# Kernel optimization log

Measured on AMD Instinct MI355X. Metric: run time of the kernel, lower is better.

## Reference

```python
import jax, jax.numpy as jnp
import numpy as np

EMB_DIM = 768
HEAD = 12
HEAD_DIM = EMB_DIM // HEAD


def setup_inputs() -> dict:
    key = jax.random.key(0)
    ks = jax.random.split(key, 6)
    B, N, D = 8, 1024, EMB_DIM
    s = 1.0 / np.sqrt(D)
    return {
        "z": jax.random.normal(ks[0], (B, N, D), dtype=jnp.float32),
        "w_q": jax.random.normal(ks[1], (D, D), dtype=jnp.float32) * s,
        "w_k": jax.random.normal(ks[2], (D, D), dtype=jnp.float32) * s,
        "w_v": jax.random.normal(ks[3], (D, D), dtype=jnp.float32) * s,
        "w_o": jax.random.normal(ks[4], (D, D), dtype=jnp.float32) * s,
        "b_o": jax.random.normal(ks[5], (D,), dtype=jnp.float32) * 0.01,
    }


def reference(z, w_q, w_k, w_v, w_o, b_o):
    B, N, D = z.shape
    sqrt_dh = jnp.asarray(HEAD_DIM, z.dtype) ** 0.5
    # project and split heads: [B, H, N, Dh]
    def heads(x, w):
        return (x @ w.T).reshape(B, N, HEAD, HEAD_DIM).transpose(0, 2, 1, 3)
    q = heads(z, w_q)
    k = heads(z, w_k)
    v = heads(z, w_v)
    dots = jnp.einsum("bhqd,bhkd->bhqk", q, k) / sqrt_dh
    attn = jax.nn.softmax(dots, axis=-1)  # dropout p=0 -> identity
    out = jnp.einsum("bhqk,bhkd->bhqd", attn, v)
    out = out.transpose(0, 2, 1, 3).reshape(B, N, D)
    return out @ w_o.T + b_o
```

## Files before the change

kernel.cpp:

```cpp
#include <hip/hip_runtime.h>
#include <hip/hip_bf16.h>
#include <stdint.h>

typedef unsigned short u16;
typedef __attribute__((ext_vector_type(8))) short bf16x8;
typedef __attribute__((ext_vector_type(4))) float f32x4;

__device__ __forceinline__ u16 f2bf(float f) {
    union { float f; unsigned int i; } c; c.f = f;
    unsigned int x = c.i;
    return (u16)((x + 0x7FFFu + ((x >> 16) & 1u)) >> 16);
}
__device__ __forceinline__ u16 f2bf_fast(float f) {
    union { float f; unsigned int i; } c; c.f = f;
    return (u16)((c.i + 0x8000u) >> 16);
}

__device__ __forceinline__ void glds16(const u16* g, u16* l) {
    __builtin_amdgcn_global_load_lds(
        (const __attribute__((address_space(1))) void*)g,
        (__attribute__((address_space(3))) void*)l, 16, 0, 0);
}

__global__ __launch_bounds__(256) void convert_all(
    const float* __restrict__ z, const float* __restrict__ wq,
    const float* __restrict__ wk, const float* __restrict__ wv,
    const float* __restrict__ wo,
    u16* __restrict__ zb, u16* __restrict__ wqb, u16* __restrict__ wkb,
    u16* __restrict__ wvb, u16* __restrict__ wob)
{
    int g = blockIdx.x * 256 + threadIdx.x;
    const float* s; u16* d;
    if (g < 786432)       { s = z;  d = zb;  }
    else if (g < 860160)  { s = wq; d = wqb; g -= 786432; }
    else if (g < 933888)  { s = wk; d = wkb; g -= 860160; }
    else if (g < 1007616) { s = wv; d = wvb; g -= 933888; }
    else                  { s = wo; d = wob; g -= 1007616; }
    float4 a = *(const float4*)(s + (size_t)g * 8);
    float4 b = *(const float4*)(s + (size_t)g * 8 + 4);
    u16 t[8] = {f2bf(a.x), f2bf(a.y), f2bf(a.z), f2bf(a.w),
                f2bf(b.x), f2bf(b.y), f2bf(b.z), f2bf(b.w)};
    *(uint4*)(d + (size_t)g * 8) = *(const uint4*)t;
}

__device__ __forceinline__ void gemm_mainloop(
    const u16* __restrict__ A, const u16* __restrict__ B,
    u16* As, u16* Bs, f32x4 (&acc)[4][4], int m0, int lda, int ldb, int K)
{
    const int t = threadIdx.x;
    const int w = t >> 6, lane = t & 63, quad = lane >> 4, lc = lane & 15;
    const int wm = w >> 1, wn = w & 1;
    const int c0 = (2 * w) * 64 + lane, c1 = c0 + 64;
    const int kq0 = c0 >> 7, row0 = c0 & 127;
    const int kq1 = c1 >> 7, row1 = c1 & 127;

    const u16* a0 = &A[(size_t)(m0 + row0) * lda + kq0 * 8];
    const u16* a1 = &A[(size_t)(m0 + row1) * lda + kq1 * 8];
    const u16* b0 = &B[(size_t)row0 * ldb + kq0 * 8];
    const u16* b1 = &B[(size_t)row1 * ldb + kq1 * 8];
    u16* la0 = &As[(2 * w) * 512];        u16* la1 = la0 + 512;
    u16* lb0 = &Bs[(2 * w) * 512];        u16* lb1 = lb0 + 512;

    glds16(a0, la0);  glds16(a1, la1);
    glds16(b0, lb0);  glds16(b1, lb1);
    __syncthreads();

    int buf = 0;
    for (int k0 = 0; k0 < K; k0 += 32) {
        if (k0 + 32 < K) {
            const int nb = (buf ^ 1) * 4096;
            glds16(a0 + k0 + 32, la0 + nb);  glds16(a1 + k0 + 32, la1 + nb);
            glds16(b0 + k0 + 32, lb0 + nb);  glds16(b1 + k0 + 32, lb1 + nb);
        }
        bf16x8 af[4], bfr[4];
        #pragma unroll
        for (int i = 0; i < 4; i++)
            af[i]  = *(const bf16x8*)&As[buf * 4096 + (quad * 128 + 64 * wm + 16 * i + lc) * 8];
        #pragma unroll
        for (int j = 0; j < 4; j++)
            bfr[j] = *(const bf16x8*)&Bs[buf * 4096 + (quad * 128 + 64 * wn + 16 * j + lc) * 8];
        #pragma unroll
        for (int i = 0; i < 4; i++)
            #pragma unroll
            for (int j = 0; j < 4; j++)
                acc[i][j] = __builtin_amdgcn_mfma_f32_16x16x32_bf16(af[i], bfr[j], acc[i][j], 0, 0, 0);
        __syncthreads();
        buf ^= 1;
    }
}

__global__ __launch_bounds__(256) void qkv_gemm(
    const u16* __restrict__ zb, const u16* __restrict__ wqb,
    const u16* __restrict__ wkb, const u16* __restrict__ wvb,
    u16* __restrict__ qkb, u16* __restrict__ vt)
{
    __shared__ __align__(16) u16 As[8192], Bs[8192];
    const int n0 = blockIdx.x * 128, m0 = blockIdx.y * 128;
    const u16* B;
    if (n0 < 768)       B = wqb + (size_t)n0 * 768;
    else if (n0 < 1536) B = wkb + (size_t)(n0 - 768) * 768;
    else                B = wvb + (size_t)(n0 - 1536) * 768;

    f32x4 acc[4][4] = {};
    gemm_mainloop(zb, B, As, Bs, acc, m0, 768, 768, 768);

    const int t = threadIdx.x;
    const int w = t >> 6, lane = t & 63, quad = lane >> 4, lc = lane & 15;
    const int wm = w >> 1, wn = w & 1;

    if (n0 < 1536) {
        #pragma unroll
        for (int i = 0; i < 4; i++)
            #pragma unroll
            for (int j = 0; j < 4; j++) {
                const int col = n0 + 64 * wn + 16 * j + lc;
                #pragma unroll
                for (int r = 0; r < 4; r++) {
                    const int row = m0 + 64 * wm + 16 * i + quad * 4 + r;
                    qkb[(size_t)row * 1536 + col] = f2bf_fast(acc[i][j][r]);
                }
            }
    } else {
        #pragma unroll
        for (int i = 0; i < 4; i++)
            #pragma unroll
            for (int j = 0; j < 4; j++) {
                const int c = (n0 - 1536) + 64 * wn + 16 * j + lc;
                const int h = c >> 6, d = c & 63;
                const int tok0 = m0 + 64 * wm + 16 * i + quad * 4;
                const int b = tok0 >> 10, n = tok0 & 1023;
                ushort4 pk = { f2bf_fast(acc[i][j][0]), f2bf_fast(acc[i][j][1]),
                               f2bf_fast(acc[i][j][2]), f2bf_fast(acc[i][j][3]) };
                *(ushort4*)&vt[(((size_t)(b * 12 + h)) * 64 + d) * 1024 + n] = pk;
            }
    }
}

__global__ __launch_bounds__(256) void oproj_gemm(
    const u16* __restrict__ ob, const u16* __restrict__ wob,
    const float* __restrict__ bo, float* __restrict__ out)
{
    __shared__ __align__(16) u16 As[8192], Bs[8192];
    const int n0 = blockIdx.x * 128, m0 = blockIdx.y * 128;
    f32x4 acc[4][4] = {};
    gemm_mainloop(ob, wob + (size_t)n0 * 768, As, Bs, acc, m0, 768, 768, 768);

    const int t = threadIdx.x;
    const int w = t >> 6, lane = t & 63, quad = lane >> 4, lc = lane & 15;
    const int wm = w >> 1, wn = w & 1;
    #pragma unroll
    for (int i = 0; i < 4; i++)
        #pragma unroll
        for (int j = 0; j < 4; j++) {
            const int col = n0 + 64 * wn + 16 * j + lc;
            const float bv = bo[col];
            #pragma unroll
            for (int r = 0; r < 4; r++) {
                const int row = m0 + 64 * wm + 16 * i + quad * 4 + r;
                out[(size_t)row * 768 + col] = acc[i][j][r] + bv;
            }
        }
}

__global__ __launch_bounds__(512, 4) void attn_kernel(
    const u16* __restrict__ qkb, const u16* __restrict__ vt,
    u16* __restrict__ obuf)
{
    const int b = blockIdx.x / 12, h = blockIdx.x % 12;
    const int q0 = blockIdx.y * 128;
    const int t = threadIdx.x;
    const int w = t >> 6, lane = t & 63, quad = lane >> 4, lc = lane & 15;

    const u16* Qp  = qkb + (size_t)b * 1024 * 1536 + h * 64;
    const u16* Kp  = Qp + 768;
    const u16* Vtp = vt + ((size_t)(b * 12 + h)) * 64 * 1024;

    __shared__ __align__(16) u16 U[128 * 136];
    __shared__ __align__(16) u16 Vts[64 * 128];

    bf16x8 qf[2];
    #pragma unroll
    for (int kk = 0; kk < 2; kk++)
        qf[kk] = *(const bf16x8*)&Qp[(size_t)(q0 + 16 * w + lc) * 1536 + kk * 32 + quad * 8];

    f32x4 oacc[4] = {};
    float lsum[4] = {0.0f, 0.0f, 0.0f, 0.0f};

    const float cs = 0.18033688011112042f;

    for (int kt = 0; kt < 8; kt++) {
        const int kb = kt * 128;
        __syncthreads();
        #pragma unroll
        for (int s2 = 0; s2 < 2; s2++) {
            const int s = 2 * w + s2;
            const int c = s * 64 + lane;
            const int kq = c >> 7, row = c & 127;
            glds16(&Kp[(size_t)(kb + row) * 1536 + kq * 8], &U[s * 512]);
        }
        #pragma unroll
        for (int s2 = 0; s2 < 2; s2++) {
            const int s = 2 * w + s2;
            const int c = s * 64 + lane;
            const int d = c >> 4, kq = (c & 15) ^ (d & 15);
            glds16(&Vtp[(size_t)d * 1024 + kb + kq * 8], &Vts[s * 512]);
        }
        __syncthreads();

        f32x4 sacc[8] = {};
        #pragma unroll
        for (int j = 0; j < 8; j++) {
            bf16x8 kf0 = *(const bf16x8*)&U[((quad) * 128 + 16 * j + lc) * 8];
            bf16x8 kf1 = *(const bf16x8*)&U[((4 + quad) * 128 + 16 * j + lc) * 8];
            sacc[j] = __builtin_amdgcn_mfma_f32_16x16x32_bf16(qf[0], kf0, sacc[j], 0, 0, 0);
            sacc[j] = __builtin_amdgcn_mfma_f32_16x16x32_bf16(qf[1], kf1, sacc[j], 0, 0, 0);
        }
        __syncthreads();

        #pragma unroll
        for (int j = 0; j < 8; j++)
            #pragma unroll
            for (int r = 0; r < 4; r++) {
                float p = __builtin_amdgcn_exp2f(sacc[j][r] * cs);
                lsum[r] += p;
                U[(16 * w + quad * 4 + r) * 136 + 16 * j + lc] = f2bf_fast(p);
            }

        #pragma unroll
        for (int ks = 0; ks < 4; ks++) {
            bf16x8 pa = *(const bf16x8*)&U[(16 * w + lc) * 136 + ks * 32 + quad * 8];
            #pragma unroll
            for (int jd = 0; jd < 4; jd++) {
                bf16x8 vb = *(const bf16x8*)&Vts[(((16 * jd + lc) << 4) + ((ks * 4 + quad) ^ lc)) * 8];
                oacc[jd] = __builtin_amdgcn_mfma_f32_16x16x32_bf16(pa, vb, oacc[jd], 0, 0, 0);
            }
        }
    }

    #pragma unroll
    for (int off = 1; off < 16; off <<= 1)
        #pragma unroll
        for (int r = 0; r < 4; r++)
            lsum[r] += __shfl_xor(lsum[r], off, 64);

    float invl[4];
    #pragma unroll
    for (int r = 0; r < 4; r++) invl[r] = __builtin_amdgcn_rcpf(lsum[r]);
    #pragma unroll
    for (int jd = 0; jd < 4; jd++)
        #pragma unroll
        for (int r = 0; r < 4; r++) {
            const int row = q0 + 16 * w + quad * 4 + r;
            const int col = h * 64 + 16 * jd + lc;
            obuf[((size_t)b * 1024 + row) * 768 + col] = f2bf_fast(oacc[jd][r] * invl[r]);
        }
}

extern "C" void kernel_launch(void* const* d_in, const int* in_sizes, int n_in,
                              void* d_out, int out_size, void* d_ws, size_t ws_size,
                              hipStream_t stream) {
    const float* z  = (const float*)d_in[0];
    const float* wq = (const float*)d_in[1];
    const float* wk = (const float*)d_in[2];
    const float* wv = (const float*)d_in[3];
    const float* wo = (const float*)d_in[4];
    const float* bo = (const float*)d_in[5];

    u16* ws16 = (u16*)d_ws;
    u16* zb   = ws16;
    u16* wqb  = zb  + 6291456;
    u16* wkb  = wqb + 589824;
    u16* wvb  = wkb + 589824;
    u16* wob  = wvb + 589824;
    u16* vt   = wob + 589824;
    u16* qkb  = (u16*)d_out;
    u16* obuf = zb;
    float* out = (float*)d_out;

    convert_all<<<4224, 256, 0, stream>>>(z, wq, wk, wv, wo, zb, wqb, wkb, wvb, wob);
    qkv_gemm<<<dim3(18, 64), 256, 0, stream>>>(zb, wqb, wkb, wvb, qkb, vt);
    attn_kernel<<<dim3(96, 8), 512, 0, stream>>>(qkb, vt, obuf);
    oproj_gemm<<<dim3(6, 64), 256, 0, stream>>>(obuf, wob, bo, out);
}
```

Measured before the change: 233.3 us.

## Switch GEMM and attention K tiles to row-major swizzled LDS layout, halve oproj M tile

Rewrites the GEMM mainloop staging so each thread loads contiguous row chunks with an XOR swizzle on the k-quad, and reads fragments through the same swizzle. The intent is to coalesce global loads better and avoid LDS bank conflicts. The attention K tile load gets the same swizzled row-major layout. The output projection uses a 64-row M tile, doubling its grid from 384 to 768 blocks to fill the CUs better. The cost is more index arithmetic and a smaller per-block tile in oproj.

```diff
diff --git a/kernel.cpp b/kernel.cpp
--- a/kernel.cpp
+++ b/kernel.cpp
@@ -43,44 +43,65 @@
     *(uint4*)(d + (size_t)g * 8) = *(const uint4*)t;
 }
 
+template <int MI>
 __device__ __forceinline__ void gemm_mainloop(
     const u16* __restrict__ A, const u16* __restrict__ B,
-    u16* As, u16* Bs, f32x4 (&acc)[4][4], int m0, int lda, int ldb, int K)
+    u16* As, u16* Bs, f32x4 (&acc)[MI][4], int m0, int lda, int ldb, int K)
 {
     const int t = threadIdx.x;
     const int w = t >> 6, lane = t & 63, quad = lane >> 4, lc = lane & 15;
     const int wm = w >> 1, wn = w & 1;
-    const int c0 = (2 * w) * 64 + lane, c1 = c0 + 64;
-    const int kq0 = c0 >> 7, row0 = c0 & 127;
-    const int kq1 = c1 >> 7, row1 = c1 & 127;
-
-    const u16* a0 = &A[(size_t)(m0 + row0) * lda + kq0 * 8];
-    const u16* a1 = &A[(size_t)(m0 + row1) * lda + kq1 * 8];
-    const u16* b0 = &B[(size_t)row0 * ldb + kq0 * 8];
-    const u16* b1 = &B[(size_t)row1 * ldb + kq1 * 8];
-    u16* la0 = &As[(2 * w) * 512];        u16* la1 = la0 + 512;
-    u16* lb0 = &Bs[(2 * w) * 512];        u16* lb1 = lb0 + 512;
-
-    glds16(a0, la0);  glds16(a1, la1);
-    glds16(b0, lb0);  glds16(b1, lb1);
+    const int swz = (lc >> 1) & 3;
+    constexpr int NA = MI / 2;
+    constexpr int ASZ = 1024 * MI;
+
+    const u16* pa[NA]; int la[NA];
+    #pragma unroll
+    for (int j = 0; j < NA; j++) {
+        const int c = j * 256 + t;
+        const int row = c >> 2;
+        const int kq = (c & 3) ^ ((row >> 1) & 3);
+        pa[j] = &A[(size_t)(m0 + row) * lda + kq * 8];
+        la[j] = (j * 256 + w * 64) * 8;
+    }
+    const u16* pb[2]; int lb[2];
+    #pragma unroll
+    for (int j = 0; j < 2; j++) {
+        const int c = j * 256 + t;
+        const int row = c >> 2;
+        const int kq = (c & 3) ^ ((row >> 1) & 3);
+        pb[j] = &B[(size_t)row * ldb + kq * 8];
+        lb[j] = (j * 256 + w * 64) * 8;
+    }
+
+    #pragma unroll
+    for (int j = 0; j < NA; j++) glds16(pa[j], As + la[j]);
+    #pragma unroll
+    for (int j = 0; j < 2; j++) glds16(pb[j], Bs + lb[j]);
     __syncthreads();
 
     int buf = 0;
     for (int k0 = 0; k0 < K; k0 += 32) {
         if (k0 + 32 < K) {
-            const int nb = (buf ^ 1) * 4096;
-            glds16(a0 + k0 + 32, la0 + nb);  glds16(a1 + k0 + 32, la1 + nb);
-            glds16(b0 + k0 + 32, lb0 + nb);  glds16(b1 + k0 + 32, lb1 + nb);
-        }
-        bf16x8 af[4], bfr[4];
-        #pragma unroll
-        for (int i = 0; i < 4; i++)
-            af[i]  = *(const bf16x8*)&As[buf * 4096 + (quad * 128 + 64 * wm + 16 * i + lc) * 8];
-        #pragma unroll
-        for (int j = 0; j < 4; j++)
-            bfr[j] = *(const bf16x8*)&Bs[buf * 4096 + (quad * 128 + 64 * wn + 16 * j + lc) * 8];
-        #pragma unroll
-        for (int i = 0; i < 4; i++)
+            const int na = (buf ^ 1) * ASZ, nbb = (buf ^ 1) * 4096;
+            #pragma unroll
+            for (int j = 0; j < NA; j++) glds16(pa[j] + k0 + 32, As + na + la[j]);
+            #pragma unroll
+            for (int j = 0; j < 2; j++)  glds16(pb[j] + k0 + 32, Bs + nbb + lb[j]);
+        }
+        bf16x8 af[MI], bfr[4];
+        #pragma unroll
+        for (int i = 0; i < MI; i++) {
+            const int row = 32 * NA * wm + 16 * i + lc;
+            af[i] = *(const bf16x8*)&As[buf * ASZ + (row * 4 + (quad ^ swz)) * 8];
+        }
+        #pragma unroll
+        for (int j = 0; j < 4; j++) {
+            const int row = 64 * wn + 16 * j + lc;
+            bfr[j] = *(const bf16x8*)&Bs[buf * 4096 + (row * 4 + (quad ^ swz)) * 8];
+        }
+        #pragma unroll
+        for (int i = 0; i < MI; i++)
             #pragma unroll
             for (int j = 0; j < 4; j++)
                 acc[i][j] = __builtin_amdgcn_mfma_f32_16x16x32_bf16(af[i], bfr[j], acc[i][j], 0, 0, 0);
@@ -102,7 +123,7 @@
     else                B = wvb + (size_t)(n0 - 1536) * 768;
 
     f32x4 acc[4][4] = {};
-    gemm_mainloop(zb, B, As, Bs, acc, m0, 768, 768, 768);
+    gemm_mainloop<4>(zb, B, As, Bs, acc, m0, 768, 768, 768);
 
     const int t = threadIdx.x;
     const int w = t >> 6, lane = t & 63, quad = lane >> 4, lc = lane & 15;
@@ -140,23 +161,23 @@
     const u16* __restrict__ ob, const u16* __restrict__ wob,
     const float* __restrict__ bo, float* __restrict__ out)
 {
-    __shared__ __align__(16) u16 As[8192], Bs[8192];
-    const int n0 = blockIdx.x * 128, m0 = blockIdx.y * 128;
-    f32x4 acc[4][4] = {};
-    gemm_mainloop(ob, wob + (size_t)n0 * 768, As, Bs, acc, m0, 768, 768, 768);
+    __shared__ __align__(16) u16 As[4096], Bs[8192];
+    const int n0 = blockIdx.x * 128, m0 = blockIdx.y * 64;
+    f32x4 acc[2][4] = {};
+    gemm_mainloop<2>(ob, wob + (size_t)n0 * 768, As, Bs, acc, m0, 768, 768, 768);
 
     const int t = threadIdx.x;
     const int w = t >> 6, lane = t & 63, quad = lane >> 4, lc = lane & 15;
     const int wm = w >> 1, wn = w & 1;
     #pragma unroll
-    for (int i = 0; i < 4; i++)
+    for (int i = 0; i < 2; i++)
         #pragma unroll
         for (int j = 0; j < 4; j++) {
             const int col = n0 + 64 * wn + 16 * j + lc;
             const float bv = bo[col];
             #pragma unroll
             for (int r = 0; r < 4; r++) {
-                const int row = m0 + 64 * wm + 16 * i + quad * 4 + r;
+                const int row = m0 + 32 * wm + 16 * i + quad * 4 + r;
                 out[(size_t)row * 768 + col] = acc[i][j][r] + bv;
             }
         }
@@ -178,6 +199,16 @@
     __shared__ __align__(16) u16 U[128 * 136];
     __shared__ __align__(16) u16 Vts[64 * 128];
 
+    const u16* kp[2]; u16* kl[2];
+    #pragma unroll
+    for (int j = 0; j < 2; j++) {
+        const int c = j * 512 + t;
+        const int row = c >> 3;
+        const int kq = (c & 7) ^ ((row >> 1) & 7);
+        kp[j] = Kp + (size_t)row * 1536 + kq * 8;
+        kl[j] = &U[(j * 512 + w * 64) * 8];
+    }
+
     bf16x8 qf[2];
     #pragma unroll
     for (int kk = 0; kk < 2; kk++)
@@ -187,17 +218,14 @@
     float lsum[4] = {0.0f, 0.0f, 0.0f, 0.0f};
 
     const float cs = 0.18033688011112042f;
+    const int swk = (lc >> 1) & 7;
 
     for (int kt = 0; kt < 8; kt++) {
         const int kb = kt * 128;
         __syncthreads();
         #pragma unroll
-        for (int s2 = 0; s2 < 2; s2++) {
-            const int s = 2 * w + s2;
-            const int c = s * 64 + lane;
-            const int kq = c >> 7, row = c & 127;
-            glds16(&Kp[(size_t)(kb + row) * 1536 + kq * 8], &U[s * 512]);
-        }
+        for (int j = 0; j < 2; j++)
+            glds16(kp[j] + (size_t)kb * 1536, kl[j]);
         #pragma unroll
         for (int s2 = 0; s2 < 2; s2++) {
             const int s = 2 * w + s2;
@@ -210,8 +238,9 @@
         f32x4 sacc[8] = {};
         #pragma unroll
         for (int j = 0; j < 8; j++) {
-            bf16x8 kf0 = *(const bf16x8*)&U[((quad) * 128 + 16 * j + lc) * 8];
-            bf16x8 kf1 = *(const bf16x8*)&U[((4 + quad) * 128 + 16 * j + lc) * 8];
+            const int nrow = 16 * j + lc;
+            bf16x8 kf0 = *(const bf16x8*)&U[(nrow * 8 + (quad ^ swk)) * 8];
+            bf16x8 kf1 = *(const bf16x8*)&U[(nrow * 8 + ((4 + quad) ^ swk)) * 8];
             sacc[j] = __builtin_amdgcn_mfma_f32_16x16x32_bf16(qf[0], kf0, sacc[j], 0, 0, 0);
             sacc[j] = __builtin_amdgcn_mfma_f32_16x16x32_bf16(qf[1], kf1, sacc[j], 0, 0, 0);
         }
@@ -280,5 +309,5 @@
     convert_all<<<4224, 256, 0, stream>>>(z, wq, wk, wv, wo, zb, wqb, wkb, wvb, wob);
     qkv_gemm<<<dim3(18, 64), 256, 0, stream>>>(zb, wqb, wkb, wvb, qkb, vt);
     attn_kernel<<<dim3(96, 8), 512, 0, stream>>>(qkb, vt, obuf);
-    oproj_gemm<<<dim3(6, 64), 256, 0, stream>>>(obuf, wob, bo, out);
-}
+    oproj_gemm<<<dim3(6, 128), 256, 0, stream>>>(obuf, wob, bo, out);
+}
```

After: 201.2 us. 13.8% less time.
